# Kernel optimization log

Measured on AMD Instinct MI355X. Metric: run time of the kernel, lower is better.

## Reference

```python
import jax, jax.numpy as jnp
import numpy as np

B = 16384
INPUT, HID, MEM, K = 512, 1024, 1152, 2
SQ = 48  # sqrt(MEM*K)
LN_EPS = 1e-5
P_EPS = 1e-12


def setup_inputs() -> dict:
    key = jax.random.key(0)
    ks = jax.random.split(key, 16)
    def lin(k, out_d, in_d):
        bound = 1.0 / np.sqrt(in_d)
        k1, k2 = jax.random.split(k)
        W = jax.random.uniform(k1, (out_d, in_d), jnp.float32, -bound, bound)
        b = jax.random.uniform(k2, (out_d,), jnp.float32, -bound, bound)
        return W, b
    W_h, b_h = lin(ks[0], HID, MEM + HID + INPUT)        # hmi2h
    W_a, b_a = lin(ks[1], K, MEM + HID)                   # hm2alpha
    W_b, b_b = lin(ks[2], K, MEM + HID)                   # hm2beta
    W_va, b_va = lin(ks[3], 2 * SQ, MEM + HID)            # hm2v_alpha
    W_vb, b_vb = lin(ks[4], 2 * SQ, MEM + HID)            # hm2v_beta
    return {
        "input": jax.random.normal(ks[5], (B, INPUT), jnp.float32),
        "h_prev": jax.random.normal(ks[6], (B, HID), jnp.float32),
        "m_prev": jax.random.normal(ks[7], (B, MEM), jnp.float32),
        "W_h": W_h, "b_h": b_h,
        "ln_g": jnp.ones((HID,), jnp.float32), "ln_b": jnp.zeros((HID,), jnp.float32),
        "W_a": W_a, "b_a": b_a, "W_b": W_b, "b_b": b_b,
        "W_va": W_va, "b_va": b_va, "W_vb": W_vb, "b_vb": b_vb,
    }


def _layernorm(x, g, b):
    mu = jnp.mean(x, axis=-1, keepdims=True)
    var = jnp.mean(jnp.square(x - mu), axis=-1, keepdims=True)
    return (x - mu) * jax.lax.rsqrt(var + LN_EPS) * g + b


def _outer_pnorm(hm, W, b):
    # u: [B, 2*SQ] -> outer product [B, SQ, SQ] -> view [B, K, MEM], p=5 normalize on last dim
    u = hm @ W.T + b
    u1, u2 = u[:, :SQ], u[:, SQ:]
    v = (u1[:, :, None] * u2[:, None, :]).reshape(-1, K, MEM)
    norm = jnp.sum(jnp.abs(v) ** 5, axis=2, keepdims=True) ** (1.0 / 5.0)
    return v / jnp.maximum(norm, P_EPS)


def reference(input, h_prev, m_prev, W_h, b_h, ln_g, ln_b, W_a, b_a, W_b, b_b, W_va, b_va, W_vb, b_vb):
    c = jnp.concatenate([input, h_prev, m_prev], axis=1)          # [B, INPUT+HID+MEM]
    h = jax.nn.relu(_layernorm(c @ W_h.T + b_h, ln_g, ln_b))      # [B, HID]
    hm = jnp.concatenate([h, m_prev], axis=1)                     # [B, HID+MEM]
    alpha = hm @ W_a.T + b_a                                      # [B, K] (use_relu=False)
    beta = hm @ W_b.T + b_b                                       # [B, K]
    v_alpha = _outer_pnorm(hm, W_va, b_va)                        # [B, K, MEM]
    v_beta = _outer_pnorm(hm, W_vb, b_vb)                         # [B, K, MEM]
    add_mem = jnp.mean(alpha[:, :, None] * v_alpha, axis=1)       # [B, MEM]
    forget_mem = jnp.mean(beta[:, :, None] * v_beta, axis=1)      # [B, MEM]
    m = m_prev + add_mem - forget_mem
    return h, m
```

## Files before the change

kernel.cpp:

```cpp
#include <hip/hip_runtime.h>
#include <hip/hip_bf16.h>
#include <cstdint>
#include <cstddef>

#define B_ROWS 16384
#define D_IN   512
#define D_HID  1024
#define D_MEM  1152
#define D_C    2688
#define D_HM   2176
#define N_U    224

typedef __attribute__((ext_vector_type(8))) short bf16x8;
typedef __attribute__((ext_vector_type(4))) float f32x4;

static __device__ __forceinline__ unsigned short f2bf(float f) {
  unsigned u = __float_as_uint(f);
  unsigned r = u + 0x7fffu + ((u >> 16) & 1u);
  return (unsigned short)(r >> 16);
}

#define GLOAD16(g, l) __builtin_amdgcn_global_load_lds( \
    (const __attribute__((address_space(1))) void*)(g), \
    (__attribute__((address_space(3))) void*)(l), 16, 0, 0)

__global__ __launch_bounds__(256) void convert3(
    const float* __restrict__ x, const float* __restrict__ h, const float* __restrict__ m,
    unsigned short* __restrict__ xb, unsigned short* __restrict__ hb, unsigned short* __restrict__ mb) {
  const int stride = gridDim.x * blockDim.x;
  const int t0 = blockIdx.x * blockDim.x + threadIdx.x;
  const int nx = B_ROWS * D_IN / 4, nh = B_ROWS * D_HID / 4, nm = B_ROWS * D_MEM / 4;
  for (int i = t0; i < nx; i += stride) {
    float4 v = ((const float4*)x)[i];
    ushort4 o; o.x=f2bf(v.x); o.y=f2bf(v.y); o.z=f2bf(v.z); o.w=f2bf(v.w);
    ((ushort4*)xb)[i] = o;
  }
  for (int i = t0; i < nh; i += stride) {
    float4 v = ((const float4*)h)[i];
    ushort4 o; o.x=f2bf(v.x); o.y=f2bf(v.y); o.z=f2bf(v.z); o.w=f2bf(v.w);
    ((ushort4*)hb)[i] = o;
  }
  for (int i = t0; i < nm; i += stride) {
    float4 v = ((const float4*)m)[i];
    ushort4 o; o.x=f2bf(v.x); o.y=f2bf(v.y); o.z=f2bf(v.z); o.w=f2bf(v.w);
    ((ushort4*)mb)[i] = o;
  }
}

__global__ void conv_w4(const float* __restrict__ W, unsigned short* __restrict__ o, int n4) {
  for (int i = blockIdx.x*blockDim.x + threadIdx.x; i < n4; i += gridDim.x*blockDim.x) {
    float4 v = ((const float4*)W)[i];
    ushort4 u; u.x=f2bf(v.x); u.y=f2bf(v.y); u.z=f2bf(v.z); u.w=f2bf(v.w);
    ((ushort4*)o)[i] = u;
  }
}

__global__ void conv_wcat(const float* __restrict__ Wva, const float* __restrict__ Wvb,
                          const float* __restrict__ Wa, const float* __restrict__ Wb,
                          unsigned short* __restrict__ o) {
  const int n = N_U * D_HM;
  for (int i = blockIdx.x*blockDim.x + threadIdx.x; i < n; i += gridDim.x*blockDim.x) {
    int r = i / D_HM, col = i - r * D_HM;
    float v;
    if (r < 96)       v = Wva[r*D_HM + col];
    else if (r < 192) v = Wvb[(r-96)*D_HM + col];
    else if (r < 194) v = Wa[(r-192)*D_HM + col];
    else if (r < 196) v = Wb[(r-194)*D_HM + col];
    else              v = 0.f;
    o[i] = f2bf(v);
  }
}

__global__ __launch_bounds__(256, 2) void gemm1(
    const unsigned short* __restrict__ Xb,
    const unsigned short* __restrict__ Hb,
    const unsigned short* __restrict__ Mb,
    const unsigned short* __restrict__ W,
    float* __restrict__ Y) {
  __shared__ __align__(16) unsigned short As[128*32];
  __shared__ __align__(16) unsigned short Bs[128*32];
  const int tid  = threadIdx.x;
  const int lane = tid & 63;
  const int wave = tid >> 6;
  const int bm = blockIdx.x & 127;
  const int bn = blockIdx.x >> 7;
  const int wr = wave >> 1, wc = wave & 1;
  const int lr = lane & 15, kh = lane >> 4;

  f32x4 acc[4][4];
  #pragma unroll
  for (int i = 0; i < 4; ++i)
    #pragma unroll
    for (int j = 0; j < 4; ++j) acc[i][j] = (f32x4)(0.f);

  const unsigned short* Wbase = W + (size_t)(bn*128) * D_C;
  const int s0 = tid, s1 = tid + 256;
  const int ar0 = s0 >> 2, ac0 = (s0 & 3) * 8;
  const int ar1 = s1 >> 2, ac1 = (s1 & 3) * 8;

  for (int k0 = 0; k0 < D_C; k0 += 32) {
    const unsigned short* asrc; int ald, akk;
    if (k0 < 512)       { asrc = Xb; ald = D_IN;  akk = k0; }
    else if (k0 < 1536) { asrc = Hb; ald = D_HID; akk = k0 - 512; }
    else                { asrc = Mb; ald = D_MEM; akk = k0 - 1536; }
    GLOAD16(asrc + (size_t)(bm*128 + ar0)*ald + akk + ac0, As + s0*8);
    GLOAD16(asrc + (size_t)(bm*128 + ar1)*ald + akk + ac1, As + s1*8);
    GLOAD16(Wbase + (size_t)ar0*D_C + k0 + ac0, Bs + s0*8);
    GLOAD16(Wbase + (size_t)ar1*D_C + k0 + ac1, Bs + s1*8);
    __syncthreads();
    bf16x8 a[4], b[4];
    #pragma unroll
    for (int mi = 0; mi < 4; ++mi)
      a[mi] = *(const bf16x8*)(As + (wr*64 + mi*16 + lr)*32 + kh*8);
    #pragma unroll
    for (int ni = 0; ni < 4; ++ni)
      b[ni] = *(const bf16x8*)(Bs + (wc*64 + ni*16 + lr)*32 + kh*8);
    #pragma unroll
    for (int mi = 0; mi < 4; ++mi)
      #pragma unroll
      for (int ni = 0; ni < 4; ++ni)
        acc[mi][ni] = __builtin_amdgcn_mfma_f32_16x16x32_bf16(a[mi], b[ni], acc[mi][ni], 0, 0, 0);
    __syncthreads();
  }
  const int orow0 = bm*128 + wr*64;
  const int ocol0 = bn*128 + wc*64;
  #pragma unroll
  for (int mi = 0; mi < 4; ++mi)
    #pragma unroll
    for (int ni = 0; ni < 4; ++ni)
      #pragma unroll
      for (int i = 0; i < 4; ++i) {
        int r  = orow0 + mi*16 + kh*4 + i;
        int cc = ocol0 + ni*16 + lr;
        Y[(size_t)r * D_HID + cc] = acc[mi][ni][i];
      }
}

__global__ __launch_bounds__(256) void ln_relu(
    float* __restrict__ Y, const float* __restrict__ bh,
    const float* __restrict__ g, const float* __restrict__ bb,
    unsigned short* __restrict__ hmh) {
  const int row = blockIdx.x;
  const int t = threadIdx.x;
  float4 x = ((const float4*)(Y + (size_t)row * D_HID))[t];
  float4 b4 = ((const float4*)bh)[t];
  x.x += b4.x; x.y += b4.y; x.z += b4.z; x.w += b4.w;
  float s  = x.x + x.y + x.z + x.w;
  float sq = x.x*x.x + x.y*x.y + x.z*x.z + x.w*x.w;
  #pragma unroll
  for (int off = 32; off >= 1; off >>= 1) {
    s  += __shfl_down(s,  off, 64);
    sq += __shfl_down(sq, off, 64);
  }
  __shared__ float red[8];
  if ((t & 63) == 0) { red[t >> 6] = s; red[4 + (t >> 6)] = sq; }
  __syncthreads();
  float ts = red[0]+red[1]+red[2]+red[3];
  float tq = red[4]+red[5]+red[6]+red[7];
  float mu = ts * (1.f/1024.f);
  float var = tq * (1.f/1024.f) - mu*mu;
  float rstd = rsqrtf(var + 1e-5f);
  float4 g4  = ((const float4*)g)[t];
  float4 bb4 = ((const float4*)bb)[t];
  float4 o;
  o.x = fmaxf(0.f, (x.x - mu)*rstd*g4.x + bb4.x);
  o.y = fmaxf(0.f, (x.y - mu)*rstd*g4.y + bb4.y);
  o.z = fmaxf(0.f, (x.z - mu)*rstd*g4.z + bb4.z);
  o.w = fmaxf(0.f, (x.w - mu)*rstd*g4.w + bb4.w);
  ((float4*)(Y + (size_t)row * D_HID))[t] = o;
  ushort4 ob; ob.x=f2bf(o.x); ob.y=f2bf(o.y); ob.z=f2bf(o.z); ob.w=f2bf(o.w);
  *(ushort4*)(hmh + (size_t)row * D_HID + t*4) = ob;
}

__global__ __launch_bounds__(512, 1) void gemm2g(
    const unsigned short* __restrict__ Hb,
    const unsigned short* __restrict__ Mb,
    const unsigned short* __restrict__ W,
    const float* __restrict__ ba, const float* __restrict__ bbt,
    const float* __restrict__ bva, const float* __restrict__ bvb,
    const float* __restrict__ mp,
    float* __restrict__ Mo) {
  __shared__ __align__(16) char smem[896 + 57344 + 2048 + 1024 + 12288];
  float*          bias_s = (float*)smem;
  unsigned short* As     = (unsigned short*)(smem + 896);
  unsigned short* Bs     = (unsigned short*)(smem + 896 + 4096);
  float*          Us     = (float*)(smem + 896);
  float*          sm_s   = (float*)(smem + 896 + 57344);
  float*          coef_s = (float*)(smem + 896 + 57344 + 2048);
  float*          q_s    = (float*)(smem + 896 + 57344 + 3072);

  const int tid  = threadIdx.x;
  const int lane = tid & 63;
  const int wave = tid >> 6;
  const int wr = wave >> 1, wc = wave & 1;
  const int lr = lane & 15, kh = lane >> 4;
  const int bm = blockIdx.x;

  if (tid < N_U) {
    int c = tid; float v;
    if (c < 96)       v = bva[c];
    else if (c < 192) v = bvb[c - 96];
    else if (c < 194) v = ba[c - 192];
    else if (c < 196) v = bbt[c - 194];
    else              v = 0.f;
    bias_s[c] = v;
  }

  f32x4 acc[7];
  #pragma unroll
  for (int i = 0; i < 7; ++i) acc[i] = (f32x4)(0.f);

  for (int k0 = 0; k0 < D_HM; k0 += 32) {
    if (tid < 256) {
      const unsigned short* asrc; int ald, akk;
      if (k0 < 1024) { asrc = Hb; ald = D_HID; akk = k0; }
      else           { asrc = Mb; ald = D_MEM; akk = k0 - 1024; }
      GLOAD16(asrc + (size_t)(bm*64 + (tid>>2))*ald + akk + (tid&3)*8, As + tid*8);
    }
    if (tid >= 256) {
      int sb = tid - 256;
      GLOAD16(W + (size_t)(sb>>2)*D_HM + k0 + (sb&3)*8, Bs + sb*8);
    }
    {
      int sb = tid + 256;
      GLOAD16(W + (size_t)(sb>>2)*D_HM + k0 + (sb&3)*8, Bs + sb*8);
    }
    if (tid < 128) {
      int sb = tid + 768;
      GLOAD16(W + (size_t)(sb>>2)*D_HM + k0 + (sb&3)*8, Bs + sb*8);
    }
    __syncthreads();
    bf16x8 a = *(const bf16x8*)(As + (wr*16 + lr)*32 + kh*8);
    #pragma unroll
    for (int ni = 0; ni < 7; ++ni) {
      bf16x8 b = *(const bf16x8*)(Bs + (wc*112 + ni*16 + lr)*32 + kh*8);
      acc[ni] = __builtin_amdgcn_mfma_f32_16x16x32_bf16(a, b, acc[ni], 0, 0, 0);
    }
    __syncthreads();
  }

  {
    const int row = wr*16 + kh*4;
    #pragma unroll
    for (int ni = 0; ni < 7; ++ni) {
      int cc = wc*112 + ni*16 + lr;
      float bb4 = bias_s[cc];
      #pragma unroll
      for (int i = 0; i < 4; ++i)
        Us[(row + i)*N_U + cc] = acc[ni][i] + bb4;
    }
  }
  __syncthreads();

  const int gr = tid >> 3;
  const int gj = tid & 7;
  {
    const float* su = Us + gr*N_U;
    float ssum = 0.f;
    #pragma unroll 4
    for (int i = 0; i < 24; ++i) {
      float a = fabsf(su[gj*24 + i]);
      float a2 = a*a;
      ssum += a2*a2*a;
    }
    sm_s[gr*8 + gj] = ssum;
  }
  __syncthreads();
  if (gj == 0) {
    const float* sm = sm_s + gr*8;
    const float* su = Us + gr*N_U;
    float S2a = sm[2] + sm[3];
    float S2b = sm[6] + sm[7];
    float n0 = powf(sm[0]*S2a, 0.2f);
    float n1 = powf(sm[1]*S2a, 0.2f);
    float n2 = powf(sm[4]*S2b, 0.2f);
    float n3 = powf(sm[5]*S2b, 0.2f);
    coef_s[gr*4+0] = 0.5f * su[192] / fmaxf(n0, 1e-12f);
    coef_s[gr*4+1] = 0.5f * su[193] / fmaxf(n1, 1e-12f);
    coef_s[gr*4+2] = 0.5f * su[194] / fmaxf(n2, 1e-12f);
    coef_s[gr*4+3] = 0.5f * su[195] / fmaxf(n3, 1e-12f);
  }
  __syncthreads();
  {
    const float* su = Us + gr*N_U;
    const float* cf = coef_s + gr*4;
    #pragma unroll
    for (int i = 0; i < 6; ++i) {
      int mq = gj*6 + i;
      float v;
      if (mq < 24) v = cf[0]*su[mq]        + cf[1]*su[24 + mq];
      else         v = cf[2]*su[96 + mq-24] + cf[3]*su[120 + mq-24];
      q_s[gr*48 + mq] = v;
    }
  }
  __syncthreads();
  {
    const float4* mp4 = (const float4*)(mp + (size_t)(bm*64) * D_MEM);
    float4*       mo4 = (float4*)(Mo + (size_t)(bm*64) * D_MEM);
    for (int idx = tid; idx < 64*288; idx += 512) {
      int row = idx / 288;
      int p4  = idx - row*288;
      int p = p4*4;
      int rr = p/48, c = p - rr*48;
      const float* su = Us + row*N_U;
      float A0 = q_s[row*48 + rr], B0 = q_s[row*48 + 24 + rr];
      float4 m = mp4[row*288 + p4];
      float4 o;
      o.x = m.x + su[48 + c    ]*A0 - su[144 + c    ]*B0;
      o.y = m.y + su[48 + c + 1]*A0 - su[144 + c + 1]*B0;
      o.z = m.z + su[48 + c + 2]*A0 - su[144 + c + 2]*B0;
      o.w = m.w + su[48 + c + 3]*A0 - su[144 + c + 3]*B0;
      mo4[row*288 + p4] = o;
    }
  }
}

extern "C" void kernel_launch(void* const* d_in, const int* in_sizes, int n_in,
                              void* d_out, int out_size, void* d_ws, size_t ws_size,
                              hipStream_t stream) {
  const float* input  = (const float*)d_in[0];
  const float* h_prev = (const float*)d_in[1];
  const float* m_prev = (const float*)d_in[2];
  const float* W_h    = (const float*)d_in[3];
  const float* b_h    = (const float*)d_in[4];
  const float* ln_g   = (const float*)d_in[5];
  const float* ln_b   = (const float*)d_in[6];
  const float* W_a    = (const float*)d_in[7];
  const float* b_a    = (const float*)d_in[8];
  const float* W_b    = (const float*)d_in[9];
  const float* b_b    = (const float*)d_in[10];
  const float* W_va   = (const float*)d_in[11];
  const float* b_va   = (const float*)d_in[12];
  const float* W_vb   = (const float*)d_in[13];
  const float* b_vb   = (const float*)d_in[14];

  const size_t off_wh   = 0;
  const size_t off_wcat = off_wh   + (size_t)D_HID * D_C * 2;
  const size_t off_xb   = off_wcat + (size_t)N_U * D_HM * 2;
  const size_t off_hb   = off_xb   + (size_t)B_ROWS * D_IN * 2;
  const size_t off_mb   = off_hb   + (size_t)B_ROWS * D_HID * 2;
  const size_t off_hmh  = off_mb   + (size_t)B_ROWS * D_MEM * 2;
  const size_t need     = off_hmh  + (size_t)B_ROWS * D_HID * 2;
  if (ws_size < need) return;

  char* ws = (char*)d_ws;
  unsigned short* wh_bf = (unsigned short*)(ws + off_wh);
  unsigned short* wc_bf = (unsigned short*)(ws + off_wcat);
  unsigned short* xb    = (unsigned short*)(ws + off_xb);
  unsigned short* hb    = (unsigned short*)(ws + off_hb);
  unsigned short* mb    = (unsigned short*)(ws + off_mb);
  unsigned short* hmh   = (unsigned short*)(ws + off_hmh);

  float* h_out = (float*)d_out;
  float* m_out = h_out + (size_t)B_ROWS * D_HID;

  convert3 <<<2048, 256, 0, stream>>>(input, h_prev, m_prev, xb, hb, mb);
  conv_w4  <<<1024, 256, 0, stream>>>(W_h, wh_bf, (D_HID * D_C) / 4);
  conv_wcat<<<256, 256, 0, stream>>>(W_va, W_vb, W_a, W_b, wc_bf);
  gemm1    <<<1024, 256, 0, stream>>>(xb, hb, mb, wh_bf, h_out);
  ln_relu  <<<B_ROWS, 256, 0, stream>>>(h_out, b_h, ln_g, ln_b, hmh);
  gemm2g   <<<B_ROWS / 64, 512, 0, stream>>>(hmh, mb, wc_bf, b_a, b_b, b_va, b_vb, m_prev, m_out);
}
```

Before: 504.7 us.

## Merge conversion kernels, use one wave per row in LN, shrink gemm2 tiles

The three fp32-to-bf16 conversion kernels are merged into a single prep launch. The layernorm kernel now handles one row per wavefront with only shuffle reductions, which removes the shared-memory reduction and the block barrier. The second GEMM moves from 64-row, 512-thread blocks to 32-row, 256-thread blocks with less LDS. This doubles the grid and allows up to four blocks per CU to improve occupancy, at the cost of reloading the weight tile twice as often per row and of uneven column work across waves.

```diff
diff --git a/kernel.cpp b/kernel.cpp
--- a/kernel.cpp
+++ b/kernel.cpp
@@ -24,12 +24,18 @@
     (const __attribute__((address_space(1))) void*)(g), \
     (__attribute__((address_space(3))) void*)(l), 16, 0, 0)
 
-__global__ __launch_bounds__(256) void convert3(
+__global__ __launch_bounds__(256) void prep(
     const float* __restrict__ x, const float* __restrict__ h, const float* __restrict__ m,
-    unsigned short* __restrict__ xb, unsigned short* __restrict__ hb, unsigned short* __restrict__ mb) {
+    const float* __restrict__ Wh,
+    const float* __restrict__ Wva, const float* __restrict__ Wvb,
+    const float* __restrict__ Wa, const float* __restrict__ Wb,
+    unsigned short* __restrict__ xb, unsigned short* __restrict__ hb,
+    unsigned short* __restrict__ mb, unsigned short* __restrict__ whb,
+    unsigned short* __restrict__ wcb) {
   const int stride = gridDim.x * blockDim.x;
   const int t0 = blockIdx.x * blockDim.x + threadIdx.x;
   const int nx = B_ROWS * D_IN / 4, nh = B_ROWS * D_HID / 4, nm = B_ROWS * D_MEM / 4;
+  const int nw = D_HID * D_C / 4;
   for (int i = t0; i < nx; i += stride) {
     float4 v = ((const float4*)x)[i];
     ushort4 o; o.x=f2bf(v.x); o.y=f2bf(v.y); o.z=f2bf(v.z); o.w=f2bf(v.w);
@@ -45,21 +51,13 @@
     ushort4 o; o.x=f2bf(v.x); o.y=f2bf(v.y); o.z=f2bf(v.z); o.w=f2bf(v.w);
     ((ushort4*)mb)[i] = o;
   }
-}
-
-__global__ void conv_w4(const float* __restrict__ W, unsigned short* __restrict__ o, int n4) {
-  for (int i = blockIdx.x*blockDim.x + threadIdx.x; i < n4; i += gridDim.x*blockDim.x) {
-    float4 v = ((const float4*)W)[i];
-    ushort4 u; u.x=f2bf(v.x); u.y=f2bf(v.y); u.z=f2bf(v.z); u.w=f2bf(v.w);
-    ((ushort4*)o)[i] = u;
-  }
-}
-
-__global__ void conv_wcat(const float* __restrict__ Wva, const float* __restrict__ Wvb,
-                          const float* __restrict__ Wa, const float* __restrict__ Wb,
-                          unsigned short* __restrict__ o) {
-  const int n = N_U * D_HM;
-  for (int i = blockIdx.x*blockDim.x + threadIdx.x; i < n; i += gridDim.x*blockDim.x) {
+  for (int i = t0; i < nw; i += stride) {
+    float4 v = ((const float4*)Wh)[i];
+    ushort4 o; o.x=f2bf(v.x); o.y=f2bf(v.y); o.z=f2bf(v.z); o.w=f2bf(v.w);
+    ((ushort4*)whb)[i] = o;
+  }
+  const int nc = N_U * D_HM;
+  for (int i = t0; i < nc; i += stride) {
     int r = i / D_HM, col = i - r * D_HM;
     float v;
     if (r < 96)       v = Wva[r*D_HM + col];
@@ -67,7 +65,7 @@
     else if (r < 194) v = Wa[(r-192)*D_HM + col];
     else if (r < 196) v = Wb[(r-194)*D_HM + col];
     else              v = 0.f;
-    o[i] = f2bf(v);
+    wcb[i] = f2bf(v);
   }
 }
 
@@ -140,39 +138,47 @@
     float* __restrict__ Y, const float* __restrict__ bh,
     const float* __restrict__ g, const float* __restrict__ bb,
     unsigned short* __restrict__ hmh) {
-  const int row = blockIdx.x;
-  const int t = threadIdx.x;
-  float4 x = ((const float4*)(Y + (size_t)row * D_HID))[t];
-  float4 b4 = ((const float4*)bh)[t];
-  x.x += b4.x; x.y += b4.y; x.z += b4.z; x.w += b4.w;
-  float s  = x.x + x.y + x.z + x.w;
-  float sq = x.x*x.x + x.y*x.y + x.z*x.z + x.w*x.w;
+  const int row  = blockIdx.x * 4 + (threadIdx.x >> 6);
+  const int lane = threadIdx.x & 63;
+  float4* Yrow = (float4*)(Y + (size_t)row * D_HID);
+  const float4* bh4 = (const float4*)bh;
+  float4 x[4];
+  float s = 0.f, sq = 0.f;
+  #pragma unroll
+  for (int j = 0; j < 4; ++j) {
+    float4 v = Yrow[lane + 64*j];
+    float4 b4 = bh4[lane + 64*j];
+    v.x += b4.x; v.y += b4.y; v.z += b4.z; v.w += b4.w;
+    x[j] = v;
+    s  += v.x + v.y + v.z + v.w;
+    sq += v.x*v.x + v.y*v.y + v.z*v.z + v.w*v.w;
+  }
   #pragma unroll
   for (int off = 32; off >= 1; off >>= 1) {
-    s  += __shfl_down(s,  off, 64);
-    sq += __shfl_down(sq, off, 64);
-  }
-  __shared__ float red[8];
-  if ((t & 63) == 0) { red[t >> 6] = s; red[4 + (t >> 6)] = sq; }
-  __syncthreads();
-  float ts = red[0]+red[1]+red[2]+red[3];
-  float tq = red[4]+red[5]+red[6]+red[7];
-  float mu = ts * (1.f/1024.f);
-  float var = tq * (1.f/1024.f) - mu*mu;
+    s  += __shfl_xor(s,  off, 64);
+    sq += __shfl_xor(sq, off, 64);
+  }
+  float mu   = s * (1.f/1024.f);
+  float var  = sq * (1.f/1024.f) - mu*mu;
   float rstd = rsqrtf(var + 1e-5f);
-  float4 g4  = ((const float4*)g)[t];
-  float4 bb4 = ((const float4*)bb)[t];
-  float4 o;
-  o.x = fmaxf(0.f, (x.x - mu)*rstd*g4.x + bb4.x);
-  o.y = fmaxf(0.f, (x.y - mu)*rstd*g4.y + bb4.y);
-  o.z = fmaxf(0.f, (x.z - mu)*rstd*g4.z + bb4.z);
-  o.w = fmaxf(0.f, (x.w - mu)*rstd*g4.w + bb4.w);
-  ((float4*)(Y + (size_t)row * D_HID))[t] = o;
-  ushort4 ob; ob.x=f2bf(o.x); ob.y=f2bf(o.y); ob.z=f2bf(o.z); ob.w=f2bf(o.w);
-  *(ushort4*)(hmh + (size_t)row * D_HID + t*4) = ob;
-}
-
-__global__ __launch_bounds__(512, 1) void gemm2g(
+  const float4* g4p  = (const float4*)g;
+  const float4* bb4p = (const float4*)bb;
+  ushort4* hrow = (ushort4*)(hmh + (size_t)row * D_HID);
+  #pragma unroll
+  for (int j = 0; j < 4; ++j) {
+    float4 g4 = g4p[lane + 64*j], bb4 = bb4p[lane + 64*j];
+    float4 o;
+    o.x = fmaxf(0.f, (x[j].x - mu)*rstd*g4.x + bb4.x);
+    o.y = fmaxf(0.f, (x[j].y - mu)*rstd*g4.y + bb4.y);
+    o.z = fmaxf(0.f, (x[j].z - mu)*rstd*g4.z + bb4.z);
+    o.w = fmaxf(0.f, (x[j].w - mu)*rstd*g4.w + bb4.w);
+    Yrow[lane + 64*j] = o;
+    ushort4 ob; ob.x=f2bf(o.x); ob.y=f2bf(o.y); ob.z=f2bf(o.z); ob.w=f2bf(o.w);
+    hrow[lane + 64*j] = ob;
+  }
+}
+
+__global__ __launch_bounds__(256, 4) void gemm2g(
     const unsigned short* __restrict__ Hb,
     const unsigned short* __restrict__ Mb,
     const unsigned short* __restrict__ W,
@@ -180,21 +186,22 @@
     const float* __restrict__ bva, const float* __restrict__ bvb,
     const float* __restrict__ mp,
     float* __restrict__ Mo) {
-  __shared__ __align__(16) char smem[896 + 57344 + 2048 + 1024 + 12288];
+  __shared__ __align__(16) char smem[37248];
   float*          bias_s = (float*)smem;
   unsigned short* As     = (unsigned short*)(smem + 896);
-  unsigned short* Bs     = (unsigned short*)(smem + 896 + 4096);
+  unsigned short* Bs     = (unsigned short*)(smem + 896 + 2048);
   float*          Us     = (float*)(smem + 896);
-  float*          sm_s   = (float*)(smem + 896 + 57344);
-  float*          coef_s = (float*)(smem + 896 + 57344 + 2048);
-  float*          q_s    = (float*)(smem + 896 + 57344 + 3072);
+  float*          sm_s   = (float*)(smem + 896 + 28672);
+  float*          coef_s = (float*)(smem + 896 + 28672 + 1024);
+  float*          q_s    = (float*)(smem + 896 + 28672 + 1536);
 
   const int tid  = threadIdx.x;
   const int lane = tid & 63;
   const int wave = tid >> 6;
-  const int wr = wave >> 1, wc = wave & 1;
   const int lr = lane & 15, kh = lane >> 4;
   const int bm = blockIdx.x;
+  const int cs = (wave < 2) ? wave*64 : 128 + (wave-2)*48;
+  const int nf = (wave < 2) ? 4 : 3;
 
   if (tid < N_U) {
     int c = tid; float v;
@@ -206,23 +213,22 @@
     bias_s[c] = v;
   }
 
-  f32x4 acc[7];
-  #pragma unroll
-  for (int i = 0; i < 7; ++i) acc[i] = (f32x4)(0.f);
+  f32x4 acc[2][4];
+  #pragma unroll
+  for (int g = 0; g < 2; ++g)
+    #pragma unroll
+    for (int i = 0; i < 4; ++i) acc[g][i] = (f32x4)(0.f);
 
   for (int k0 = 0; k0 < D_HM; k0 += 32) {
-    if (tid < 256) {
+    if (tid < 128) {
       const unsigned short* asrc; int ald, akk;
       if (k0 < 1024) { asrc = Hb; ald = D_HID; akk = k0; }
       else           { asrc = Mb; ald = D_MEM; akk = k0 - 1024; }
-      GLOAD16(asrc + (size_t)(bm*64 + (tid>>2))*ald + akk + (tid&3)*8, As + tid*8);
-    }
-    if (tid >= 256) {
-      int sb = tid - 256;
-      GLOAD16(W + (size_t)(sb>>2)*D_HM + k0 + (sb&3)*8, Bs + sb*8);
-    }
-    {
-      int sb = tid + 256;
+      GLOAD16(asrc + (size_t)(bm*32 + (tid>>2))*ald + akk + (tid&3)*8, As + tid*8);
+    }
+    #pragma unroll
+    for (int kq = 0; kq < 3; ++kq) {
+      int sb = tid + 256*kq;
       GLOAD16(W + (size_t)(sb>>2)*D_HM + k0 + (sb&3)*8, Bs + sb*8);
     }
     if (tid < 128) {
@@ -230,24 +236,31 @@
       GLOAD16(W + (size_t)(sb>>2)*D_HM + k0 + (sb&3)*8, Bs + sb*8);
     }
     __syncthreads();
-    bf16x8 a = *(const bf16x8*)(As + (wr*16 + lr)*32 + kh*8);
-    #pragma unroll
-    for (int ni = 0; ni < 7; ++ni) {
-      bf16x8 b = *(const bf16x8*)(Bs + (wc*112 + ni*16 + lr)*32 + kh*8);
-      acc[ni] = __builtin_amdgcn_mfma_f32_16x16x32_bf16(a, b, acc[ni], 0, 0, 0);
+    bf16x8 a0 = *(const bf16x8*)(As + (lr)*32 + kh*8);
+    bf16x8 a1 = *(const bf16x8*)(As + (16 + lr)*32 + kh*8);
+    #pragma unroll
+    for (int ni = 0; ni < 4; ++ni) {
+      if (ni < nf) {
+        bf16x8 b = *(const bf16x8*)(Bs + (cs + ni*16 + lr)*32 + kh*8);
+        acc[0][ni] = __builtin_amdgcn_mfma_f32_16x16x32_bf16(a0, b, acc[0][ni], 0, 0, 0);
+        acc[1][ni] = __builtin_amdgcn_mfma_f32_16x16x32_bf16(a1, b, acc[1][ni], 0, 0, 0);
+      }
     }
     __syncthreads();
   }
 
-  {
-    const int row = wr*16 + kh*4;
-    #pragma unroll
-    for (int ni = 0; ni < 7; ++ni) {
-      int cc = wc*112 + ni*16 + lr;
-      float bb4 = bias_s[cc];
+  #pragma unroll
+  for (int ni = 0; ni < 4; ++ni) {
+    if (ni < nf) {
+      int cc = cs + ni*16 + lr;
+      float bv = bias_s[cc];
       #pragma unroll
-      for (int i = 0; i < 4; ++i)
-        Us[(row + i)*N_U + cc] = acc[ni][i] + bb4;
+      for (int g = 0; g < 2; ++g) {
+        int row = g*16 + kh*4;
+        #pragma unroll
+        for (int i = 0; i < 4; ++i)
+          Us[(row + i)*N_U + cc] = acc[g][ni][i] + bv;
+      }
     }
   }
   __syncthreads();
@@ -288,16 +301,16 @@
     for (int i = 0; i < 6; ++i) {
       int mq = gj*6 + i;
       float v;
-      if (mq < 24) v = cf[0]*su[mq]        + cf[1]*su[24 + mq];
+      if (mq < 24) v = cf[0]*su[mq]         + cf[1]*su[24 + mq];
       else         v = cf[2]*su[96 + mq-24] + cf[3]*su[120 + mq-24];
       q_s[gr*48 + mq] = v;
     }
   }
   __syncthreads();
   {
-    const float4* mp4 = (const float4*)(mp + (size_t)(bm*64) * D_MEM);
-    float4*       mo4 = (float4*)(Mo + (size_t)(bm*64) * D_MEM);
-    for (int idx = tid; idx < 64*288; idx += 512) {
+    const float4* mp4 = (const float4*)(mp + (size_t)(bm*32) * D_MEM);
+    float4*       mo4 = (float4*)(Mo + (size_t)(bm*32) * D_MEM);
+    for (int idx = tid; idx < 32*288; idx += 256) {
       int row = idx / 288;
       int p4  = idx - row*288;
       int p = p4*4;
@@ -354,10 +367,10 @@
   float* h_out = (float*)d_out;
   float* m_out = h_out + (size_t)B_ROWS * D_HID;
 
-  convert3 <<<2048, 256, 0, stream>>>(input, h_prev, m_prev, xb, hb, mb);
-  conv_w4  <<<1024, 256, 0, stream>>>(W_h, wh_bf, (D_HID * D_C) / 4);
-  conv_wcat<<<256, 256, 0, stream>>>(W_va, W_vb, W_a, W_b, wc_bf);
-  gemm1    <<<1024, 256, 0, stream>>>(xb, hb, mb, wh_bf, h_out);
-  ln_relu  <<<B_ROWS, 256, 0, stream>>>(h_out, b_h, ln_g, ln_b, hmh);
-  gemm2g   <<<B_ROWS / 64, 512, 0, stream>>>(hmh, mb, wc_bf, b_a, b_b, b_va, b_vb, m_prev, m_out);
-}
+  prep   <<<2048, 256, 0, stream>>>(input, h_prev, m_prev, W_h,
+                                    W_va, W_vb, W_a, W_b,
+                                    xb, hb, mb, wh_bf, wc_bf);
+  gemm1  <<<1024, 256, 0, stream>>>(xb, hb, mb, wh_bf, h_out);
+  ln_relu<<<B_ROWS / 4, 256, 0, stream>>>(h_out, b_h, ln_g, ln_b, hmh);
+  gemm2g <<<B_ROWS / 32, 256, 0, stream>>>(hmh, mb, wc_bf, b_a, b_b, b_va, b_vb, m_prev, m_out);
+}
```

New measurement: 484.6 us. 4.0% less time.
